# Kernel tuning notes

Measured on AMD Instinct MI355X. Metric: run time of the kernel, lower is better.

## Reference

```python
import jax, jax.numpy as jnp
import numpy as np

EMBED = 1024
HEADS = 16
HEAD_DIM = EMBED // HEADS


def setup_inputs() -> dict:
    key = jax.random.key(0)
    ks = jax.random.split(key, 6)
    N, S, E = 2, 2048, EMBED
    value = jax.random.normal(ks[0], (N, S, E), dtype=jnp.float32)
    k = jax.random.normal(ks[1], (N, S, E), dtype=jnp.float32)
    q = jax.random.normal(ks[2], (N, S, E), dtype=jnp.float32)
    mask = jax.random.randint(ks[3], (N, 1, S, S), 0, 2, dtype=jnp.int32)
    W_fc = jax.random.normal(ks[4], (E, E), dtype=jnp.float32) * (1.0 / np.sqrt(E))
    b_fc = jax.random.normal(ks[5], (E,), dtype=jnp.float32) * 0.01
    return {"value": value, "key": k, "query": q, "mask": mask, "W_fc": W_fc, "b_fc": b_fc}


def reference(value, key, query, mask, W_fc, b_fc):
    N, Sq, E = query.shape
    Sk = key.shape[1]
    Sv = value.shape[1]
    # NOTE: the original module never applies its q/k/v Linear layers (source bug);
    # it only reshapes into heads.
    v = value.reshape(N, Sv, HEADS, HEAD_DIM)
    k = key.reshape(N, Sk, HEADS, HEAD_DIM)
    q = query.reshape(N, Sq, HEADS, HEAD_DIM)
    # energy: [N, H, Q, K]
    energy = jnp.einsum('nqhd,nkhd->nhqk', q, k)
    energy = jnp.where(mask == 0, jnp.float32(-1e20), energy)
    # scale by sqrt(embed_size) as in the source (not sqrt(head_dim))
    attention = jax.nn.softmax(energy / jnp.sqrt(jnp.float32(E)), axis=3)
    out = jnp.einsum('nhql,nlhd->nqhd', attention, v).reshape(N, Sq, E)
    # torch Linear: x @ W.T + b
    out = out @ W_fc.T + b_fc
    return out
```

## Files before the change

### kernel.cpp

```cpp
#include <hip/hip_runtime.h>
#include <hip/hip_bf16.h>
#include <math.h>

#define S_LEN 2048
#define EMB   1024
#define HEADS 16
#define HDIM  64
#define SPLIT 4

#define C_SCALE   0.045084439f
#define BIAS_OK  -2.0f

#define NE  ((size_t)2 * S_LEN * EMB)
#define NL  ((size_t)2 * S_LEN * HEADS)
#define NMB ((size_t)2 * S_LEN * S_LEN / 64)

typedef __bf16 bf16x8 __attribute__((ext_vector_type(8)));
typedef float  f32x4  __attribute__((ext_vector_type(4)));

__device__ __forceinline__ bf16x8 cvt8(const float* v) {
    bf16x8 r;
#pragma unroll
    for (int i = 0; i < 8; ++i) r[i] = (__bf16)v[i];
    return r;
}
__device__ __forceinline__ unsigned long long pack4(float a, float b, float c, float d) {
    __bf16 t[4] = {(__bf16)a, (__bf16)b, (__bf16)c, (__bf16)d};
    return *(unsigned long long*)t;
}
__device__ __forceinline__ void gld_lds16(const void* g, void* l) {
    __builtin_amdgcn_global_load_lds(
        (const __attribute__((address_space(1))) void*)g,
        (__attribute__((address_space(3))) void*)l, 16, 0, 0);
}

__global__ __launch_bounds__(256)
void prepass_kernel(const float* __restrict__ Wf, const int* __restrict__ Mp,
                    __bf16* __restrict__ Wb, unsigned long long* __restrict__ Mb) {
    const int bid = blockIdx.x, tid = threadIdx.x;
    if (bid < 512) {
        size_t i = ((size_t)bid * 256 + tid) * 8;
        float t[8];
        *(float4*)&t[0] = *(const float4*)(Wf + i);
        *(float4*)&t[4] = *(const float4*)(Wf + i + 4);
        *(bf16x8*)(Wb + i) = cvt8(t);
    } else {
        const int w = tid >> 6, lane = tid & 63;
        const int wave = (bid - 512) * 4 + w;
#pragma unroll 4
        for (int it = 0; it < 16; ++it) {
            size_t chunk = (size_t)wave * 16 + it;
            int4 v = *(const int4*)(Mp + chunk * 256 + lane * 4);
            unsigned long long b0 = __ballot(v.x != 0);
            unsigned long long b1 = __ballot(v.y != 0);
            unsigned long long b2 = __ballot(v.z != 0);
            unsigned long long b3 = __ballot(v.w != 0);
            if (lane < 4) {
                int sh = lane * 16;
                unsigned long long wv = ((b0 >> sh) & 0xFFFFULL)
                                      | (((b1 >> sh) & 0xFFFFULL) << 16)
                                      | (((b2 >> sh) & 0xFFFFULL) << 32)
                                      | (((b3 >> sh) & 0xFFFFULL) << 48);
                Mb[chunk * 4 + lane] = wv;
            }
        }
    }
}

__global__ __launch_bounds__(256)
void attn_kernel(const float* __restrict__ Vp, const float* __restrict__ Kp,
                 const float* __restrict__ Qp, const unsigned long long* __restrict__ Mb,
                 __bf16* __restrict__ Opart, float* __restrict__ Lpart) {
    __shared__ __bf16 Klds[64 * 64];
    __shared__ __bf16 Vtlds[64 * 64];
    __shared__ __bf16 Plds[4][16 * 64];

    const int tid  = threadIdx.x;
    const int lane = tid & 63;
    const int w    = tid >> 6;
    const int nblk = 2 * HEADS * SPLIT * 16;
    const int bid  = (blockIdx.x & 7) * (nblk / 8) + (blockIdx.x >> 3);
    const int qt = bid & 15;
    const int sp = (bid >> 4) & (SPLIT - 1);
    const int h  = (bid >> 6) & 15;
    const int n  = bid >> 10;

    const int ql = lane & 15;
    const int g  = lane >> 4;

    const float* qbase = Qp + (size_t)n * S_LEN * EMB + h * HDIM;
    const float* kbase = Kp + (size_t)n * S_LEN * EMB + h * HDIM;
    const float* vbase = Vp + (size_t)n * S_LEN * EMB + h * HDIM;

    const int qw = qt * 128 + w * 32;

    bf16x8 qfrag[2][2];
#pragma unroll
    for (int qf = 0; qf < 2; ++qf) {
        const float* qp = qbase + (size_t)(qw + qf * 16 + ql) * EMB + g * 8;
#pragma unroll
        for (int ks = 0; ks < 2; ++ks) {
            float tmp[8];
            *(float4*)&tmp[0] = *(const float4*)(qp + ks * 32);
            *(float4*)&tmp[4] = *(const float4*)(qp + ks * 32 + 4);
            qfrag[qf][ks] = cvt8(tmp);
        }
    }

    f32x4 oacc[2][4] = {};
    f32x4 lacc[2] = {};
    bf16x8 aon;
#pragma unroll
    for (int i = 0; i < 8; ++i) aon[i] = (__bf16)1.0f;

    const unsigned long long* mb0 = Mb + ((size_t)(n * S_LEN + qw + ql) << 5);
    const unsigned long long* mb1 = Mb + ((size_t)(n * S_LEN + qw + 16 + ql) << 5);

    const int sk  = tid >> 2;
    const int sdq = (tid & 3) * 16;
    const int d0  = (tid & 31) * 2;
    const int kv8 = (tid >> 5) * 8;

    const int kvbase = sp * (S_LEN / SPLIT);
    const int niter  = (S_LEN / SPLIT) / 64;

#pragma unroll 1
    for (int t = 0; t < niter; ++t) {
        const int kv0 = kvbase + t * 64;
        __syncthreads();
        {
            const float* kp = kbase + (size_t)(kv0 + sk) * EMB + sdq;
            float tk[16];
            *(float4*)&tk[0]  = *(const float4*)kp;
            *(float4*)&tk[4]  = *(const float4*)(kp + 4);
            *(float4*)&tk[8]  = *(const float4*)(kp + 8);
            *(float4*)&tk[12] = *(const float4*)(kp + 12);
            *(bf16x8*)((char*)Klds + sk * 128 + ((sdq * 2)       ^ ((sk & 7) << 4))) = cvt8(&tk[0]);
            *(bf16x8*)((char*)Klds + sk * 128 + (((sdq + 8) * 2) ^ ((sk & 7) << 4))) = cvt8(&tk[8]);

            const float* vp = vbase + (size_t)(kv0 + kv8) * EMB + d0;
            float r0[8], r1[8];
#pragma unroll
            for (int j = 0; j < 8; ++j) {
                float2 tv = *(const float2*)(vp + (size_t)j * EMB);
                r0[j] = tv.x; r1[j] = tv.y;
            }
            *(bf16x8*)((char*)Vtlds + d0 * 128       + ((kv8 * 2) ^ ((d0 & 7) << 4)))       = cvt8(r0);
            *(bf16x8*)((char*)Vtlds + (d0 + 1) * 128 + ((kv8 * 2) ^ (((d0 + 1) & 7) << 4))) = cvt8(r1);
        }
        __syncthreads();

        f32x4 e[4][2];
        __builtin_amdgcn_s_setprio(1);
#pragma unroll
        for (int jt = 0; jt < 4; ++jt) {
            int row = jt * 16 + ql;
            bf16x8 k0 = *(const bf16x8*)((char*)Klds + row * 128 + ((g * 16)      ^ ((row & 7) << 4)));
            bf16x8 k1 = *(const bf16x8*)((char*)Klds + row * 128 + ((64 + g * 16) ^ ((row & 7) << 4)));
#pragma unroll
            for (int qf = 0; qf < 2; ++qf) {
                f32x4 z = {};
                z         = __builtin_amdgcn_mfma_f32_16x16x32_bf16(k0, qfrag[qf][0], z, 0, 0, 0);
                e[jt][qf] = __builtin_amdgcn_mfma_f32_16x16x32_bf16(k1, qfrag[qf][1], z, 0, 0, 0);
            }
        }
        __builtin_amdgcn_s_setprio(0);

        bf16x8 pf[2][2];
#pragma unroll
        for (int qf = 0; qf < 2; ++qf) {
            const unsigned long long m64 = (qf ? mb1 : mb0)[(kv0 >> 6)];
            const unsigned u  = (unsigned)(m64 >> g);
            const unsigned uh = (unsigned)(m64 >> (g + 32));
#pragma unroll
            for (int jt = 0; jt < 4; ++jt) {
                float mb_0 = (float)((u  >> (jt * 4))      & 1u);
                float mb_1 = (float)((u  >> (jt * 4 + 16)) & 1u);
                float mb_2 = (float)((uh >> (jt * 4))      & 1u);
                float mb_3 = (float)((uh >> (jt * 4 + 16)) & 1u);
                float p0 = __builtin_amdgcn_exp2f(fmaf(e[jt][qf][0], C_SCALE, BIAS_OK)) * mb_0;
                float p1 = __builtin_amdgcn_exp2f(fmaf(e[jt][qf][1], C_SCALE, BIAS_OK)) * mb_1;
                float p2 = __builtin_amdgcn_exp2f(fmaf(e[jt][qf][2], C_SCALE, BIAS_OK)) * mb_2;
                float p3 = __builtin_amdgcn_exp2f(fmaf(e[jt][qf][3], C_SCALE, BIAS_OK)) * mb_3;
                *(unsigned long long*)((char*)Plds[w] + ql * 128 +
                    ((jt * 32 + g * 8) ^ ((ql & 7) << 4))) = pack4(p0, p1, p2, p3);
            }
#pragma unroll
            for (int ks = 0; ks < 2; ++ks)
                pf[ks][qf] = *(const bf16x8*)((char*)Plds[w] + ql * 128 +
                    ((ks * 64 + g * 16) ^ ((ql & 7) << 4)));
            lacc[qf] = __builtin_amdgcn_mfma_f32_16x16x32_bf16(aon, pf[0][qf], lacc[qf], 0, 0, 0);
            lacc[qf] = __builtin_amdgcn_mfma_f32_16x16x32_bf16(aon, pf[1][qf], lacc[qf], 0, 0, 0);
        }

        __builtin_amdgcn_s_setprio(1);
#pragma unroll
        for (int dt = 0; dt < 4; ++dt) {
            int row = dt * 16 + ql;
            bf16x8 v0 = *(const bf16x8*)((char*)Vtlds + row * 128 + ((g * 16)      ^ ((row & 7) << 4)));
            bf16x8 v1 = *(const bf16x8*)((char*)Vtlds + row * 128 + ((64 + g * 16) ^ ((row & 7) << 4)));
#pragma unroll
            for (int qf = 0; qf < 2; ++qf) {
                oacc[qf][dt] = __builtin_amdgcn_mfma_f32_16x16x32_bf16(v0, pf[0][qf], oacc[qf][dt], 0, 0, 0);
                oacc[qf][dt] = __builtin_amdgcn_mfma_f32_16x16x32_bf16(v1, pf[1][qf], oacc[qf][dt], 0, 0, 0);
            }
        }
        __builtin_amdgcn_s_setprio(0);
    }

#pragma unroll
    for (int qf = 0; qf < 2; ++qf) {
        const int q = qw + qf * 16 + ql;
        __bf16* op = Opart + (size_t)sp * NE + ((size_t)n * S_LEN + q) * EMB + h * HDIM;
#pragma unroll
        for (int dt = 0; dt < 4; ++dt)
            *(unsigned long long*)(op + dt * 16 + g * 4) =
                pack4(oacc[qf][dt][0], oacc[qf][dt][1], oacc[qf][dt][2], oacc[qf][dt][3]);
        if (g == 0)
            Lpart[(size_t)sp * NL + ((size_t)n * S_LEN + q) * HEADS + h] = lacc[qf][0];
    }
}

__global__ __launch_bounds__(256)
void reduce_kernel(const __bf16* __restrict__ Opart, const float* __restrict__ Lpart,
                   __bf16* __restrict__ X) {
    size_t e0 = ((size_t)blockIdx.x * 256 + threadIdx.x) * 8;
    size_t hr = e0 >> 6;
    float l = 0.f;
#pragma unroll
    for (int s = 0; s < SPLIT; ++s) l += Lpart[s * NL + hr];
    float inv = 1.f / l;
    float acc[8] = {};
#pragma unroll
    for (int s = 0; s < SPLIT; ++s) {
        bf16x8 v = *(const bf16x8*)(Opart + s * NE + e0);
#pragma unroll
        for (int i = 0; i < 8; ++i) acc[i] += (float)v[i];
    }
    bf16x8 r;
#pragma unroll
    for (int i = 0; i < 8; ++i) r[i] = (__bf16)(acc[i] * inv);
    *(bf16x8*)(X + e0) = r;
}

__global__ __launch_bounds__(256)
void fc_kernel(const __bf16* __restrict__ X, const __bf16* __restrict__ Wb,
               const float* __restrict__ bfc, float* __restrict__ Out) {
    __shared__ __bf16 Al[128 * 32];
    __shared__ __bf16 Bl[128 * 32];
    const int tid = threadIdx.x, lane = tid & 63, w = tid >> 6;
    const int ql = lane & 15, g = lane >> 4;
    const int bm = blockIdx.x >> 3, bn = blockIdx.x & 7;
    const int wr = w >> 1, wc = w & 1;

    const int rowL = lane >> 2;
    const int colE = (lane & 3) * 8;

    f32x4 acc[4][4] = {};

    for (int k0 = 0; k0 < EMB; k0 += 32) {
        __syncthreads();
        const int q0 = w * 2, q1 = w * 2 + 1;
        gld_lds16(X  + (size_t)(bm * 128 + q0 * 16 + rowL) * EMB + k0 + colE, Al + q0 * 512);
        gld_lds16(X  + (size_t)(bm * 128 + q1 * 16 + rowL) * EMB + k0 + colE, Al + q1 * 512);
        gld_lds16(Wb + (size_t)(bn * 128 + q0 * 16 + rowL) * EMB + k0 + colE, Bl + q0 * 512);
        gld_lds16(Wb + (size_t)(bn * 128 + q1 * 16 + rowL) * EMB + k0 + colE, Bl + q1 * 512);
        __syncthreads();

        bf16x8 a[4], b[4];
#pragma unroll
        for (int mi = 0; mi < 4; ++mi)
            a[mi] = *(const bf16x8*)(Al + (wr * 64 + mi * 16 + ql) * 32 + g * 8);
#pragma unroll
        for (int nj = 0; nj < 4; ++nj)
            b[nj] = *(const bf16x8*)(Bl + (wc * 64 + nj * 16 + ql) * 32 + g * 8);
#pragma unroll
        for (int mi = 0; mi < 4; ++mi)
#pragma unroll
            for (int nj = 0; nj < 4; ++nj)
                acc[mi][nj] = __builtin_amdgcn_mfma_f32_16x16x32_bf16(a[mi], b[nj], acc[mi][nj], 0, 0, 0);
    }

#pragma unroll
    for (int nj = 0; nj < 4; ++nj) {
        int col = bn * 128 + wc * 64 + nj * 16 + ql;
        float bias = bfc[col];
#pragma unroll
        for (int mi = 0; mi < 4; ++mi) {
            int row0 = bm * 128 + wr * 64 + mi * 16 + g * 4;
#pragma unroll
            for (int r = 0; r < 4; ++r)
                Out[(size_t)(row0 + r) * EMB + col] = acc[mi][nj][r] + bias;
        }
    }
}

extern "C" void kernel_launch(void* const* d_in, const int* in_sizes, int n_in,
                              void* d_out, int out_size, void* d_ws, size_t ws_size,
                              hipStream_t stream) {
    const float* Vp = (const float*)d_in[0];
    const float* Kp = (const float*)d_in[1];
    const float* Qp = (const float*)d_in[2];
    const int*   Mp = (const int*)d_in[3];
    const float* Wf = (const float*)d_in[4];
    const float* bf = (const float*)d_in[5];
    float* Out = (float*)d_out;

    char* p = (char*)d_ws;
    __bf16* Opart = (__bf16*)p;             p += SPLIT * NE * 2;
    float*  Lpart = (float*)p;              p += SPLIT * NL * 4;
    __bf16* Wb    = (__bf16*)p;             p += (size_t)EMB * EMB * 2;
    unsigned long long* Mb = (unsigned long long*)p;

    prepass_kernel<<<dim3(1024), dim3(256), 0, stream>>>(Wf, Mp, Wb, Mb);
    attn_kernel<<<dim3(2 * HEADS * SPLIT * 16), dim3(256), 0, stream>>>(Vp, Kp, Qp, Mb, Opart, Lpart);
    reduce_kernel<<<dim3(NE / 8 / 256), dim3(256), 0, stream>>>(Opart, Lpart, Opart);
    fc_kernel<<<dim3((2 * S_LEN / 128) * (EMB / 128)), dim3(256), 0, stream>>>(Opart, Wb, bf, Out);
}
```

Baseline: 128.3 us.

## Switch attention to 32x32x16 MFMA with register-shuffled P and row-wise mask bits

Rewrites the attention inner loop to use 32x32x16 bf16 MFMA tiles, with each wave covering 32 query rows. The probability tile is rebuilt in registers via a cross-half-wave shuffle instead of a round trip through LDS. The row sum is now plain VALU adds rather than ones-vector MFMAs. The mask prepass is changed to a simple per-row 64-bit ballot layout that matches the new fragment mapping, and launch bounds request 4 blocks per CU, which trades LDS traffic and extra MFMAs for shuffles and register pressure.

```diff
diff --git a/kernel.cpp b/kernel.cpp
--- a/kernel.cpp
+++ b/kernel.cpp
@@ -17,6 +17,7 @@
 
 typedef __bf16 bf16x8 __attribute__((ext_vector_type(8)));
 typedef float  f32x4  __attribute__((ext_vector_type(4)));
+typedef float  f32x16 __attribute__((ext_vector_type(16)));
 
 __device__ __forceinline__ bf16x8 cvt8(const float* v) {
     bf16x8 r;
@@ -27,6 +28,10 @@
 __device__ __forceinline__ unsigned long long pack4(float a, float b, float c, float d) {
     __bf16 t[4] = {(__bf16)a, (__bf16)b, (__bf16)c, (__bf16)d};
     return *(unsigned long long*)t;
+}
+__device__ __forceinline__ bf16x8 cat2(unsigned long long lo, unsigned long long hi) {
+    unsigned long long t[2] = {lo, hi};
+    return *(bf16x8*)t;
 }
 __device__ __forceinline__ void gld_lds16(const void* g, void* l) {
     __builtin_amdgcn_global_load_lds(
@@ -46,34 +51,23 @@
         *(bf16x8*)(Wb + i) = cvt8(t);
     } else {
         const int w = tid >> 6, lane = tid & 63;
-        const int wave = (bid - 512) * 4 + w;
+        const int wg = (bid - 512) * 4 + w;
 #pragma unroll 4
-        for (int it = 0; it < 16; ++it) {
-            size_t chunk = (size_t)wave * 16 + it;
-            int4 v = *(const int4*)(Mp + chunk * 256 + lane * 4);
-            unsigned long long b0 = __ballot(v.x != 0);
-            unsigned long long b1 = __ballot(v.y != 0);
-            unsigned long long b2 = __ballot(v.z != 0);
-            unsigned long long b3 = __ballot(v.w != 0);
-            if (lane < 4) {
-                int sh = lane * 16;
-                unsigned long long wv = ((b0 >> sh) & 0xFFFFULL)
-                                      | (((b1 >> sh) & 0xFFFFULL) << 16)
-                                      | (((b2 >> sh) & 0xFFFFULL) << 32)
-                                      | (((b3 >> sh) & 0xFFFFULL) << 48);
-                Mb[chunk * 4 + lane] = wv;
-            }
-        }
-    }
-}
-
-__global__ __launch_bounds__(256)
+        for (int it = 0; it < 64; ++it) {
+            size_t W = (size_t)wg * 64 + it;
+            int v = Mp[W * 64 + lane];
+            unsigned long long b = __ballot(v != 0);
+            if (lane == 0) Mb[W] = b;
+        }
+    }
+}
+
+__global__ __launch_bounds__(256, 4)
 void attn_kernel(const float* __restrict__ Vp, const float* __restrict__ Kp,
                  const float* __restrict__ Qp, const unsigned long long* __restrict__ Mb,
                  __bf16* __restrict__ Opart, float* __restrict__ Lpart) {
     __shared__ __bf16 Klds[64 * 64];
     __shared__ __bf16 Vtlds[64 * 64];
-    __shared__ __bf16 Plds[4][16 * 64];
 
     const int tid  = threadIdx.x;
     const int lane = tid & 63;
@@ -85,36 +79,29 @@
     const int h  = (bid >> 6) & 15;
     const int n  = bid >> 10;
 
-    const int ql = lane & 15;
-    const int g  = lane >> 4;
+    const int ql = lane & 31;
+    const int g  = lane >> 5;
 
     const float* qbase = Qp + (size_t)n * S_LEN * EMB + h * HDIM;
     const float* kbase = Kp + (size_t)n * S_LEN * EMB + h * HDIM;
     const float* vbase = Vp + (size_t)n * S_LEN * EMB + h * HDIM;
 
-    const int qw = qt * 128 + w * 32;
-
-    bf16x8 qfrag[2][2];
-#pragma unroll
-    for (int qf = 0; qf < 2; ++qf) {
-        const float* qp = qbase + (size_t)(qw + qf * 16 + ql) * EMB + g * 8;
-#pragma unroll
-        for (int ks = 0; ks < 2; ++ks) {
-            float tmp[8];
-            *(float4*)&tmp[0] = *(const float4*)(qp + ks * 32);
-            *(float4*)&tmp[4] = *(const float4*)(qp + ks * 32 + 4);
-            qfrag[qf][ks] = cvt8(tmp);
-        }
-    }
-
-    f32x4 oacc[2][4] = {};
-    f32x4 lacc[2] = {};
-    bf16x8 aon;
-#pragma unroll
-    for (int i = 0; i < 8; ++i) aon[i] = (__bf16)1.0f;
-
-    const unsigned long long* mb0 = Mb + ((size_t)(n * S_LEN + qw + ql) << 5);
-    const unsigned long long* mb1 = Mb + ((size_t)(n * S_LEN + qw + 16 + ql) << 5);
+    const int q = qt * 128 + w * 32 + ql;
+
+    bf16x8 qfrag[4];
+#pragma unroll
+    for (int ds_ = 0; ds_ < 4; ++ds_) {
+        const float* qp = qbase + (size_t)q * EMB + ds_ * 16 + g * 8;
+        float tmp[8];
+        *(float4*)&tmp[0] = *(const float4*)qp;
+        *(float4*)&tmp[4] = *(const float4*)(qp + 4);
+        qfrag[ds_] = cvt8(tmp);
+    }
+
+    f32x16 oacc[2] = {};
+    float la = 0.f;
+
+    const unsigned long long* mrow = Mb + ((size_t)(n * S_LEN + q) << 5);
 
     const int sk  = tid >> 2;
     const int sdq = (tid & 3) * 16;
@@ -150,75 +137,66 @@
         }
         __syncthreads();
 
-        f32x4 e[4][2];
-        __builtin_amdgcn_s_setprio(1);
-#pragma unroll
-        for (int jt = 0; jt < 4; ++jt) {
-            int row = jt * 16 + ql;
-            bf16x8 k0 = *(const bf16x8*)((char*)Klds + row * 128 + ((g * 16)      ^ ((row & 7) << 4)));
-            bf16x8 k1 = *(const bf16x8*)((char*)Klds + row * 128 + ((64 + g * 16) ^ ((row & 7) << 4)));
-#pragma unroll
-            for (int qf = 0; qf < 2; ++qf) {
-                f32x4 z = {};
-                z         = __builtin_amdgcn_mfma_f32_16x16x32_bf16(k0, qfrag[qf][0], z, 0, 0, 0);
-                e[jt][qf] = __builtin_amdgcn_mfma_f32_16x16x32_bf16(k1, qfrag[qf][1], z, 0, 0, 0);
-            }
-        }
-        __builtin_amdgcn_s_setprio(0);
-
-        bf16x8 pf[2][2];
-#pragma unroll
-        for (int qf = 0; qf < 2; ++qf) {
-            const unsigned long long m64 = (qf ? mb1 : mb0)[(kv0 >> 6)];
-            const unsigned u  = (unsigned)(m64 >> g);
-            const unsigned uh = (unsigned)(m64 >> (g + 32));
-#pragma unroll
-            for (int jt = 0; jt < 4; ++jt) {
-                float mb_0 = (float)((u  >> (jt * 4))      & 1u);
-                float mb_1 = (float)((u  >> (jt * 4 + 16)) & 1u);
-                float mb_2 = (float)((uh >> (jt * 4))      & 1u);
-                float mb_3 = (float)((uh >> (jt * 4 + 16)) & 1u);
-                float p0 = __builtin_amdgcn_exp2f(fmaf(e[jt][qf][0], C_SCALE, BIAS_OK)) * mb_0;
-                float p1 = __builtin_amdgcn_exp2f(fmaf(e[jt][qf][1], C_SCALE, BIAS_OK)) * mb_1;
-                float p2 = __builtin_amdgcn_exp2f(fmaf(e[jt][qf][2], C_SCALE, BIAS_OK)) * mb_2;
-                float p3 = __builtin_amdgcn_exp2f(fmaf(e[jt][qf][3], C_SCALE, BIAS_OK)) * mb_3;
-                *(unsigned long long*)((char*)Plds[w] + ql * 128 +
-                    ((jt * 32 + g * 8) ^ ((ql & 7) << 4))) = pack4(p0, p1, p2, p3);
-            }
-#pragma unroll
-            for (int ks = 0; ks < 2; ++ks)
-                pf[ks][qf] = *(const bf16x8*)((char*)Plds[w] + ql * 128 +
-                    ((ks * 64 + g * 16) ^ ((ql & 7) << 4)));
-            lacc[qf] = __builtin_amdgcn_mfma_f32_16x16x32_bf16(aon, pf[0][qf], lacc[qf], 0, 0, 0);
-            lacc[qf] = __builtin_amdgcn_mfma_f32_16x16x32_bf16(aon, pf[1][qf], lacc[qf], 0, 0, 0);
-        }
-
-        __builtin_amdgcn_s_setprio(1);
-#pragma unroll
-        for (int dt = 0; dt < 4; ++dt) {
-            int row = dt * 16 + ql;
-            bf16x8 v0 = *(const bf16x8*)((char*)Vtlds + row * 128 + ((g * 16)      ^ ((row & 7) << 4)));
-            bf16x8 v1 = *(const bf16x8*)((char*)Vtlds + row * 128 + ((64 + g * 16) ^ ((row & 7) << 4)));
-#pragma unroll
-            for (int qf = 0; qf < 2; ++qf) {
-                oacc[qf][dt] = __builtin_amdgcn_mfma_f32_16x16x32_bf16(v0, pf[0][qf], oacc[qf][dt], 0, 0, 0);
-                oacc[qf][dt] = __builtin_amdgcn_mfma_f32_16x16x32_bf16(v1, pf[1][qf], oacc[qf][dt], 0, 0, 0);
-            }
-        }
-        __builtin_amdgcn_s_setprio(0);
-    }
-
-#pragma unroll
-    for (int qf = 0; qf < 2; ++qf) {
-        const int q = qw + qf * 16 + ql;
-        __bf16* op = Opart + (size_t)sp * NE + ((size_t)n * S_LEN + q) * EMB + h * HDIM;
-#pragma unroll
-        for (int dt = 0; dt < 4; ++dt)
-            *(unsigned long long*)(op + dt * 16 + g * 4) =
-                pack4(oacc[qf][dt][0], oacc[qf][dt][1], oacc[qf][dt][2], oacc[qf][dt][3]);
-        if (g == 0)
-            Lpart[(size_t)sp * NL + ((size_t)n * S_LEN + q) * HEADS + h] = lacc[qf][0];
-    }
+        const unsigned long long m64 = mrow[kv0 >> 6];
+
+#pragma unroll
+        for (int kt = 0; kt < 2; ++kt) {
+            f32x16 E = {};
+            __builtin_amdgcn_s_setprio(1);
+#pragma unroll
+            for (int ds_ = 0; ds_ < 4; ++ds_) {
+                int row = kt * 32 + ql;
+                bf16x8 kf = *(const bf16x8*)((char*)Klds + row * 128 +
+                    ((ds_ * 32 + g * 16) ^ ((row & 7) << 4)));
+                E = __builtin_amdgcn_mfma_f32_32x32x16_bf16(kf, qfrag[ds_], E, 0, 0, 0);
+            }
+            __builtin_amdgcn_s_setprio(0);
+
+            const unsigned u = (unsigned)(m64 >> (kt * 32 + 4 * g));
+            unsigned long long own[4];
+#pragma unroll
+            for (int rq = 0; rq < 4; ++rq) {
+                unsigned nib = u >> (8 * rq);
+                float p0 = __builtin_amdgcn_exp2f(fmaf(E[4*rq+0], C_SCALE, BIAS_OK)) * (float)(nib & 1u);
+                float p1 = __builtin_amdgcn_exp2f(fmaf(E[4*rq+1], C_SCALE, BIAS_OK)) * (float)((nib >> 1) & 1u);
+                float p2 = __builtin_amdgcn_exp2f(fmaf(E[4*rq+2], C_SCALE, BIAS_OK)) * (float)((nib >> 2) & 1u);
+                float p3 = __builtin_amdgcn_exp2f(fmaf(E[4*rq+3], C_SCALE, BIAS_OK)) * (float)((nib >> 3) & 1u);
+                la += (p0 + p1) + (p2 + p3);
+                own[rq] = pack4(p0, p1, p2, p3);
+            }
+
+            unsigned long long sa = g ? own[0] : own[1];
+            unsigned long long sb = g ? own[2] : own[3];
+            unsigned long long ra = __shfl_xor((long long)sa, 32);
+            unsigned long long rb = __shfl_xor((long long)sb, 32);
+            bf16x8 frag0 = g ? cat2(ra, own[1]) : cat2(own[0], ra);
+            bf16x8 frag1 = g ? cat2(rb, own[3]) : cat2(own[2], rb);
+
+            __builtin_amdgcn_s_setprio(1);
+#pragma unroll
+            for (int dt = 0; dt < 2; ++dt) {
+                int row = dt * 32 + ql;
+                bf16x8 v0 = *(const bf16x8*)((char*)Vtlds + row * 128 +
+                    (((2*kt) * 32 + g * 16) ^ ((row & 7) << 4)));
+                bf16x8 v1 = *(const bf16x8*)((char*)Vtlds + row * 128 +
+                    (((2*kt+1) * 32 + g * 16) ^ ((row & 7) << 4)));
+                oacc[dt] = __builtin_amdgcn_mfma_f32_32x32x16_bf16(v0, frag0, oacc[dt], 0, 0, 0);
+                oacc[dt] = __builtin_amdgcn_mfma_f32_32x32x16_bf16(v1, frag1, oacc[dt], 0, 0, 0);
+            }
+            __builtin_amdgcn_s_setprio(0);
+        }
+    }
+
+    float lt = la + __shfl_xor(la, 32);
+    __bf16* op = Opart + (size_t)sp * NE + ((size_t)n * S_LEN + q) * EMB + h * HDIM;
+#pragma unroll
+    for (int dt = 0; dt < 2; ++dt)
+#pragma unroll
+        for (int rq = 0; rq < 4; ++rq)
+            *(unsigned long long*)(op + dt * 32 + 8 * rq + 4 * g) =
+                pack4(oacc[dt][4*rq], oacc[dt][4*rq+1], oacc[dt][4*rq+2], oacc[dt][4*rq+3]);
+    if (g == 0)
+        Lpart[(size_t)sp * NL + ((size_t)n * S_LEN + q) * HEADS + h] = lt;
 }
 
 __global__ __launch_bounds__(256)
```

Measured after the change: 131.3 us. +2.4%, slower.
